# Optimization experiments

Hardware: AMD Instinct MI355X
Metric: run time of the kernel (lower is better)

## Reference

```python
import jax, jax.numpy as jnp
import numpy as np

N = 50000
E = 625000
D_IN, D_HID, D_OUT = 128, 128, 64


def setup_inputs() -> dict:
    key = jax.random.key(0)
    k1, k2, k3, k4 = jax.random.split(key, 4)
    x = jax.random.normal(k1, (N, D_IN), dtype=jnp.float32)
    edge_index = jax.random.randint(k2, (2, E), 0, N, dtype=jnp.int32)
    # Glorot-ish init for linear weights (PyG lin has no bias; bias added after agg)
    W1 = jax.random.normal(k3, (D_HID, D_IN), dtype=jnp.float32) / np.sqrt(D_IN)
    b1 = jnp.zeros((D_HID,), dtype=jnp.float32)
    W2 = jax.random.normal(k4, (D_OUT, D_HID), dtype=jnp.float32) / np.sqrt(D_HID)
    b2 = jnp.zeros((D_OUT,), dtype=jnp.float32)
    return {"x": x, "edge_index": edge_index, "W1": W1, "b1": b1, "W2": W2, "b2": b2}


def _gcn_conv(x, W, b, src, dst, n):
    # GCNConv: h = x @ W^T; out[dst] += norm * h[src]; out += b
    # src/dst already include self-loops; symmetric normalization deg^{-1/2}.
    ones = jnp.ones(src.shape[0], dtype=x.dtype)
    deg = jax.ops.segment_sum(ones, dst, num_segments=n)
    dinv = jnp.where(deg > 0, jax.lax.rsqrt(deg), 0.0)
    norm = dinv[src] * dinv[dst]                      # [E+N]
    h = x @ W.T                                        # [N, d_out]
    msg = norm[:, None] * h[src]                       # [E+N, d_out]
    out = jax.ops.segment_sum(msg, dst, num_segments=n)
    return out + b


def reference(x, edge_index, W1, b1, W2, b2):
    n = x.shape[0]
    loops = jnp.arange(n, dtype=edge_index.dtype)
    src = jnp.concatenate([edge_index[0], loops])      # add self-loops
    dst = jnp.concatenate([edge_index[1], loops])
    h = _gcn_conv(x, W1, b1, src, dst, n)
    h = jax.nn.relu(h)
    out = _gcn_conv(h, W2, b2, src, dst, n)
    return out
```

## Files before the change

### kernel.cpp

```cpp
#include <hip/hip_runtime.h>
#include <hip/hip_bf16.h>


typedef __attribute__((ext_vector_type(8))) __bf16 bf16x8;
typedef __attribute__((ext_vector_type(8))) unsigned short ushort8;
typedef __attribute__((ext_vector_type(4))) float floatx4;

static __device__ __forceinline__ float bf2f(unsigned short s) {
    unsigned u = ((unsigned)s) << 16;
    return __builtin_bit_cast(float, u);
}
static __device__ __forceinline__ unsigned short f2bf(float f) {
    unsigned u = __builtin_bit_cast(unsigned, f);
    unsigned r = (u + 0x7FFFu + ((u >> 16) & 1u)) >> 16;
    return (unsigned short)r;
}
static __device__ __forceinline__ void ld8f(const void* p, size_t idx, int isbf, float* o) {
    if (isbf) {
        ushort8 t = __builtin_bit_cast(ushort8, *(const int4*)((const unsigned short*)p + idx));
        #pragma unroll
        for (int j = 0; j < 8; ++j) o[j] = bf2f(t[j]);
    } else {
        const float* f = (const float*)p + idx;
        float4 a = *(const float4*)f;
        float4 b = *(const float4*)(f + 4);
        o[0]=a.x; o[1]=a.y; o[2]=a.z; o[3]=a.w; o[4]=b.x; o[5]=b.y; o[6]=b.z; o[7]=b.w;
    }
}
static __device__ __forceinline__ int4 ld8frag(const void* p, size_t idx, int isbf) {
    if (isbf) {
        return *(const int4*)((const unsigned short*)p + idx);
    } else {
        const float* f = (const float*)p + idx;
        float4 a = *(const float4*)f;
        float4 b = *(const float4*)(f + 4);
        ushort8 t;
        t[0]=f2bf(a.x); t[1]=f2bf(a.y); t[2]=f2bf(a.z); t[3]=f2bf(a.w);
        t[4]=f2bf(b.x); t[5]=f2bf(b.y); t[6]=f2bf(b.z); t[7]=f2bf(b.w);
        return __builtin_bit_cast(int4, t);
    }
}
static __device__ __forceinline__ float bread(const void* p, int i, int isbf) {
    return isbf ? bf2f(((const unsigned short*)p)[i]) : ((const float*)p)[i];
}

__global__ __launch_bounds__(256) void k_countdet(
    const int* __restrict__ dst, int* __restrict__ cnt, int E, int EB,
    const unsigned* __restrict__ xw, int* __restrict__ flag)
{
    int b = blockIdx.x;
    if (b == EB) {
        __shared__ int red[256];
        int t = threadIdx.x;
        int c = 0;
        #pragma unroll
        for (int i = 0; i < 16; ++i) {
            unsigned w = xw[t * 16 + i];
            unsigned exp = (w >> 7) & 0xFFu;
            c += (exp <= 0x84u) ? 1 : 0;
        }
        red[t] = c;
        __syncthreads();
        for (int s = 128; s > 0; s >>= 1) {
            if (t < s) red[t] += red[t + s];
            __syncthreads();
        }
        if (t == 0) flag[0] = (red[0] >= 3686) ? 1 : 0;
        return;
    }
    int e = b * 256 + threadIdx.x;
    if (e < E) atomicAdd(&cnt[dst[e]], 1);
}

__global__ __launch_bounds__(256) void k_scanA(
    const int* __restrict__ cnt, int* __restrict__ partial, int N)
{
    int b = blockIdx.x, t = threadIdx.x;
    int base = b * 1024 + t * 4;
    int s = 0;
    if (base + 3 < N) {
        int4 v = *(const int4*)&cnt[base];
        s = v.x + v.y + v.z + v.w;
    } else {
        for (int j = 0; j < 4; ++j) { int i = base + j; if (i < N) s += cnt[i]; }
    }
    #pragma unroll
    for (int d = 1; d < 64; d <<= 1) s += __shfl_down(s, d, 64);
    __shared__ int ws[4];
    int lane = t & 63, wid = t >> 6;
    if (lane == 0) ws[wid] = s;
    __syncthreads();
    if (t == 0) partial[b] = ws[0] + ws[1] + ws[2] + ws[3];
}

__global__ __launch_bounds__(256) void k_scanC(
    const int* __restrict__ cnt, const int* __restrict__ partial,
    int* __restrict__ off, int* __restrict__ cursor, float* __restrict__ dinv,
    int N, int nb)
{
    __shared__ int s_pref, s_tot;
    int b = blockIdx.x, t = threadIdx.x, lane = t & 63, wid = t >> 6;
    if (t == 0) {
        int s = 0, pb = 0;
        for (int i = 0; i < nb; ++i) { if (i == b) pb = s; s += partial[i]; }
        s_pref = pb; s_tot = s;
    }
    int base = b * 1024 + t * 4;
    int v[4], s = 0;
    #pragma unroll
    for (int j = 0; j < 4; ++j) {
        int i = base + j;
        v[j] = (i < N) ? cnt[i] : 0;
        s += v[j];
    }
    int x = s;
    #pragma unroll
    for (int d = 1; d < 64; d <<= 1) {
        int u = __shfl_up(x, d, 64);
        if (lane >= d) x += u;
    }
    __shared__ int wtot[4], woff[4];
    if (lane == 63) wtot[wid] = x;
    __syncthreads();
    if (t == 0) {
        int a = 0;
        #pragma unroll
        for (int w = 0; w < 4; ++w) { woff[w] = a; a += wtot[w]; }
    }
    __syncthreads();
    int excl = s_pref + woff[wid] + (x - s);
    #pragma unroll
    for (int j = 0; j < 4; ++j) {
        int i = base + j;
        if (i < N) {
            off[i] = excl;
            cursor[i] = excl;
            dinv[i] = rsqrtf(1.0f + (float)v[j]);
            excl += v[j];
        }
    }
    if (b == 0 && t == 0) off[N] = s_tot;
}

__global__ void k_scatter(const int* __restrict__ src, const int* __restrict__ dst,
                          const float* __restrict__ dinv,
                          int* __restrict__ cursor, int2* __restrict__ bucket, int E) {
    int e = blockIdx.x * 256 + threadIdx.x;
    if (e >= E) return;
    int s = src[e], d = dst[e];
    float w = dinv[s] * dinv[d];
    int pos = atomicAdd(&cursor[d], 1);
    int2 rec; rec.x = s; rec.y = __builtin_bit_cast(int, w);
    bucket[pos] = rec;
}

__global__ __launch_bounds__(256) void k_gather1(
    const void* __restrict__ x, const float* __restrict__ dinv,
    const int* __restrict__ off, const int2* __restrict__ bucket,
    unsigned short* __restrict__ z1, int N, const int* __restrict__ flag)
{
    int isbf = *flag;
    int gid = blockIdx.x * 256 + threadIdx.x;
    int node = gid >> 4, p = gid & 15;
    if (node >= N) return;
    float di = dinv[node];
    float acc[8], va[8], vb[8];
    ld8f(x, (size_t)node * 128 + p * 8, isbf, va);
    float w0 = di * di;
    #pragma unroll
    for (int j = 0; j < 8; ++j) acc[j] = w0 * va[j];
    int it = off[node], s1 = off[node + 1];
    for (; it + 1 < s1; it += 2) {
        int2 ea = bucket[it], eb = bucket[it + 1];
        float wa = __builtin_bit_cast(float, ea.y);
        float wb = __builtin_bit_cast(float, eb.y);
        ld8f(x, (size_t)ea.x * 128 + p * 8, isbf, va);
        ld8f(x, (size_t)eb.x * 128 + p * 8, isbf, vb);
        #pragma unroll
        for (int j = 0; j < 8; ++j) acc[j] += wa * va[j] + wb * vb[j];
    }
    if (it < s1) {
        int2 ea = bucket[it];
        float wa = __builtin_bit_cast(float, ea.y);
        ld8f(x, (size_t)ea.x * 128 + p * 8, isbf, va);
        #pragma unroll
        for (int j = 0; j < 8; ++j) acc[j] += wa * va[j];
    }
    ushort8 o;
    #pragma unroll
    for (int j = 0; j < 8; ++j) o[j] = f2bf(acc[j]);
    *(int4*)&z1[(size_t)node * 128 + p * 8] = __builtin_bit_cast(int4, o);
}

__global__ __launch_bounds__(256) void k_gemm12(
    const unsigned short* __restrict__ z1, const void* __restrict__ W1,
    const void* __restrict__ b1, const void* __restrict__ W2,
    unsigned short* __restrict__ h2, int N, const int* __restrict__ flag)
{
    int isbf = *flag;
    __shared__ int4 w1f[2048];
    __shared__ unsigned short h1t[4][16 * 136];
    int tid = threadIdx.x;
    for (int u = tid; u < 2048; u += 256) {
        int nt = u >> 8, kt = (u >> 6) & 3, lane = u & 63;
        int so = (nt * 16 + (lane & 15)) * 128 + kt * 32 + ((lane >> 4) << 3);
        w1f[u] = ld8frag(W1, so, isbf);
    }
    int wave = tid >> 6, lane = tid & 63, m = lane & 15, quad = lane >> 4;

    int4 w2r[4][4];
    #pragma unroll
    for (int nt = 0; nt < 4; ++nt)
        #pragma unroll
        for (int kt = 0; kt < 4; ++kt)
            w2r[nt][kt] = ld8frag(W2, (nt * 16 + m) * 128 + kt * 32 + quad * 8, isbf);
    __syncthreads();

    int ntile = (N + 15) >> 4;
    int tile = blockIdx.x * 4 + wave;
    int tcl = (tile < ntile) ? tile : (ntile - 1);
    int arow = tcl * 16 + m;
    if (arow >= N) arow = N - 1;

    bf16x8 a[4];
    #pragma unroll
    for (int kt = 0; kt < 4; ++kt)
        a[kt] = __builtin_bit_cast(bf16x8, *(const int4*)&z1[(size_t)arow * 128 + kt * 32 + quad * 8]);
    floatx4 acc[8];
    floatx4 z = {0.f, 0.f, 0.f, 0.f};
    #pragma unroll
    for (int nt = 0; nt < 8; ++nt) acc[nt] = z;
    #pragma unroll
    for (int kt = 0; kt < 4; ++kt)
        #pragma unroll
        for (int nt = 0; nt < 8; ++nt) {
            bf16x8 b = __builtin_bit_cast(bf16x8, w1f[nt * 256 + kt * 64 + lane]);
            acc[nt] = __builtin_amdgcn_mfma_f32_16x16x32_bf16(a[kt], b, acc[nt], 0, 0, 0);
        }
    #pragma unroll
    for (int nt = 0; nt < 8; ++nt) {
        int col = nt * 16 + m;
        float bb = bread(b1, col, isbf);
        #pragma unroll
        for (int r = 0; r < 4; ++r) {
            float v = acc[nt][r] + bb;
            h1t[wave][(quad * 4 + r) * 136 + col] = f2bf(fmaxf(v, 0.f));
        }
    }
    __syncthreads();

    bf16x8 a2[4];
    #pragma unroll
    for (int kt = 0; kt < 4; ++kt)
        a2[kt] = __builtin_bit_cast(bf16x8, *(const int4*)&h1t[wave][m * 136 + kt * 32 + quad * 8]);
    floatx4 acc2[4];
    #pragma unroll
    for (int nt = 0; nt < 4; ++nt) acc2[nt] = z;
    #pragma unroll
    for (int kt = 0; kt < 4; ++kt)
        #pragma unroll
        for (int nt = 0; nt < 4; ++nt) {
            bf16x8 b = __builtin_bit_cast(bf16x8, w2r[nt][kt]);
            acc2[nt] = __builtin_amdgcn_mfma_f32_16x16x32_bf16(a2[kt], b, acc2[nt], 0, 0, 0);
        }
    if (tile < ntile) {
        int rbase = tcl * 16 + quad * 4;
        #pragma unroll
        for (int nt = 0; nt < 4; ++nt) {
            int col = nt * 16 + m;
            #pragma unroll
            for (int r = 0; r < 4; ++r) {
                int orow = rbase + r;
                if (orow < N)
                    h2[(size_t)orow * 64 + col] = f2bf(acc2[nt][r]);
            }
        }
    }
}

__global__ __launch_bounds__(256) void k_gather2(
    const unsigned short* __restrict__ h2, const float* __restrict__ dinv,
    const int* __restrict__ off, const int2* __restrict__ bucket,
    const void* __restrict__ b2, void* __restrict__ out, int N,
    const int* __restrict__ flag)
{
    int isbf = *flag;
    int gid = blockIdx.x * 256 + threadIdx.x;
    int node = gid >> 3, p = gid & 7;
    if (node >= N) return;
    float di = dinv[node];
    float acc[8];
    {
        ushort8 t = __builtin_bit_cast(ushort8, *(const int4*)&h2[(size_t)node * 64 + p * 8]);
        float w0 = di * di;
        #pragma unroll
        for (int j = 0; j < 8; ++j) acc[j] = w0 * bf2f(t[j]);
    }
    int it = off[node], s1 = off[node + 1];
    for (; it + 1 < s1; it += 2) {
        int2 ea = bucket[it], eb = bucket[it + 1];
        float wa = __builtin_bit_cast(float, ea.y);
        float wb = __builtin_bit_cast(float, eb.y);
        ushort8 ta = __builtin_bit_cast(ushort8, *(const int4*)&h2[(size_t)ea.x * 64 + p * 8]);
        ushort8 tb = __builtin_bit_cast(ushort8, *(const int4*)&h2[(size_t)eb.x * 64 + p * 8]);
        #pragma unroll
        for (int j = 0; j < 8; ++j) acc[j] += wa * bf2f(ta[j]) + wb * bf2f(tb[j]);
    }
    if (it < s1) {
        int2 ea = bucket[it];
        float wa = __builtin_bit_cast(float, ea.y);
        ushort8 ta = __builtin_bit_cast(ushort8, *(const int4*)&h2[(size_t)ea.x * 64 + p * 8]);
        #pragma unroll
        for (int j = 0; j < 8; ++j) acc[j] += wa * bf2f(ta[j]);
    }
    #pragma unroll
    for (int j = 0; j < 8; ++j) acc[j] += bread(b2, p * 8 + j, isbf);
    if (isbf) {
        ushort8 o;
        #pragma unroll
        for (int j = 0; j < 8; ++j) o[j] = f2bf(acc[j]);
        *(int4*)((unsigned short*)out + (size_t)node * 64 + p * 8) = __builtin_bit_cast(int4, o);
    } else {
        float* fo = (float*)out + (size_t)node * 64 + p * 8;
        float4 a = {acc[0], acc[1], acc[2], acc[3]};
        float4 b = {acc[4], acc[5], acc[6], acc[7]};
        *(float4*)fo = a;
        *(float4*)(fo + 4) = b;
    }
}

extern "C" void kernel_launch(void* const* d_in, const int* in_sizes, int n_in,
                              void* d_out, int out_size, void* d_ws, size_t ws_size,
                              hipStream_t stream) {
    const void* x  = d_in[0];
    const int*  ei = (const int*)d_in[1];
    const void* W1 = d_in[2];
    const void* b1 = d_in[3];
    const void* W2 = d_in[4];
    const void* b2 = d_in[5];

    int N = in_sizes[0] / 128;
    int E = in_sizes[1] / 2;
    const int* srcI = ei;
    const int* dstI = ei + E;

    int nb = (N + 1023) / 1024;
    int EB = (E + 255) / 256;

    char* base = (char*)d_ws;
    size_t o = 0;
    auto take = [&](size_t bytes) { size_t r = o; o += (bytes + 255) & ~(size_t)255; return r; };
    int*   flag    = (int*)  (base + take(4));
    int*   cnt     = (int*)  (base + take((size_t)N * 4));
    int*   off     = (int*)  (base + take((size_t)(N + 1) * 4));
    int*   cursor  = (int*)  (base + take((size_t)N * 4));
    float* dinv    = (float*)(base + take((size_t)N * 4));
    int*   partial = (int*)  (base + take((size_t)nb * 4));
    int2*  bucket  = (int2*) (base + take((size_t)E * 8));
    unsigned short* z1 = (unsigned short*)(base + take((size_t)N * 128 * 2));
    unsigned short* h2 = (unsigned short*)(base + take((size_t)N * 64 * 2));

    int ntile = (N + 15) / 16;
    int gemmBlocks = (ntile + 3) / 4;

    hipMemsetAsync(cnt, 0, (size_t)N * 4, stream);
    k_countdet<<<EB + 1, 256, 0, stream>>>(dstI, cnt, E, EB, (const unsigned*)x, flag);
    k_scanA<<<nb, 256, 0, stream>>>(cnt, partial, N);
    k_scanC<<<nb, 256, 0, stream>>>(cnt, partial, off, cursor, dinv, N, nb);
    k_scatter<<<EB, 256, 0, stream>>>(srcI, dstI, dinv, cursor, bucket, E);
    k_gather1<<<(N * 16 + 255) / 256, 256, 0, stream>>>(x, dinv, off, bucket, z1, N, flag);
    k_gemm12<<<gemmBlocks, 256, 0, stream>>>(z1, W1, b1, W2, h2, N, flag);
    k_gather2<<<(N * 8 + 255) / 256, 256, 0, stream>>>(h2, dinv, off, bucket, b2, d_out, N, flag);
}
```

Measured before the change: 250.5 us.

## Partially sort CSR neighbor lists by source quartile for gather locality

Counts and bucket positions are now kept per (destination, source-quartile) pair, so each node's neighbor list is grouped into four source-index ranges. The intent is that concurrent gathers across nodes touch nearby source rows at the same time, improving L2 locality for the feature reads in both gather kernels. In exchange the count, offset and cursor arrays grow fourfold, the scan processes four times as many entries, and every edge pays an integer division.

Result: faster. 244.4 us (-2.4%).

```diff
diff --git a/kernel.cpp b/kernel.cpp
--- a/kernel.cpp
+++ b/kernel.cpp
@@ -45,7 +45,8 @@
 }
 
 __global__ __launch_bounds__(256) void k_countdet(
-    const int* __restrict__ dst, int* __restrict__ cnt, int E, int EB,
+    const int* __restrict__ src, const int* __restrict__ dst,
+    int* __restrict__ cnt, int E, int EB, int qdiv,
     const unsigned* __restrict__ xw, int* __restrict__ flag)
 {
     int b = blockIdx.x;
@@ -69,20 +70,24 @@
         return;
     }
     int e = b * 256 + threadIdx.x;
-    if (e < E) atomicAdd(&cnt[dst[e]], 1);
+    if (e < E) {
+        int s = src[e], d = dst[e];
+        int q = s / qdiv; q = (q > 3) ? 3 : q;
+        atomicAdd(&cnt[d * 4 + q], 1);
+    }
 }
 
 __global__ __launch_bounds__(256) void k_scanA(
-    const int* __restrict__ cnt, int* __restrict__ partial, int N)
+    const int* __restrict__ cnt, int* __restrict__ partial, int M)
 {
     int b = blockIdx.x, t = threadIdx.x;
     int base = b * 1024 + t * 4;
     int s = 0;
-    if (base + 3 < N) {
+    if (base + 3 < M) {
         int4 v = *(const int4*)&cnt[base];
         s = v.x + v.y + v.z + v.w;
     } else {
-        for (int j = 0; j < 4; ++j) { int i = base + j; if (i < N) s += cnt[i]; }
+        for (int j = 0; j < 4; ++j) { int i = base + j; if (i < M) s += cnt[i]; }
     }
     #pragma unroll
     for (int d = 1; d < 64; d <<= 1) s += __shfl_down(s, d, 64);
@@ -96,7 +101,7 @@
 __global__ __launch_bounds__(256) void k_scanC(
     const int* __restrict__ cnt, const int* __restrict__ partial,
     int* __restrict__ off, int* __restrict__ cursor, float* __restrict__ dinv,
-    int N, int nb)
+    int M, int nb)
 {
     __shared__ int s_pref, s_tot;
     int b = blockIdx.x, t = threadIdx.x, lane = t & 63, wid = t >> 6;
@@ -110,7 +115,7 @@
     #pragma unroll
     for (int j = 0; j < 4; ++j) {
         int i = base + j;
-        v[j] = (i < N) ? cnt[i] : 0;
+        v[j] = (i < M) ? cnt[i] : 0;
         s += v[j];
     }
     int x = s;
@@ -132,24 +137,29 @@
     #pragma unroll
     for (int j = 0; j < 4; ++j) {
         int i = base + j;
-        if (i < N) {
+        if (i < M) {
             off[i] = excl;
             cursor[i] = excl;
-            dinv[i] = rsqrtf(1.0f + (float)v[j]);
             excl += v[j];
         }
     }
-    if (b == 0 && t == 0) off[N] = s_tot;
+    if (base < M) {
+        int node = base >> 2;
+        dinv[node] = rsqrtf(1.0f + (float)s);
+    }
+    if (b == 0 && t == 0) off[M] = s_tot;
 }
 
 __global__ void k_scatter(const int* __restrict__ src, const int* __restrict__ dst,
                           const float* __restrict__ dinv,
-                          int* __restrict__ cursor, int2* __restrict__ bucket, int E) {
+                          int* __restrict__ cursor, int2* __restrict__ bucket,
+                          int E, int qdiv) {
     int e = blockIdx.x * 256 + threadIdx.x;
     if (e >= E) return;
     int s = src[e], d = dst[e];
+    int q = s / qdiv; q = (q > 3) ? 3 : q;
     float w = dinv[s] * dinv[d];
-    int pos = atomicAdd(&cursor[d], 1);
+    int pos = atomicAdd(&cursor[d * 4 + q], 1);
     int2 rec; rec.x = s; rec.y = __builtin_bit_cast(int, w);
     bucket[pos] = rec;
 }
@@ -169,7 +179,7 @@
     float w0 = di * di;
     #pragma unroll
     for (int j = 0; j < 8; ++j) acc[j] = w0 * va[j];
-    int it = off[node], s1 = off[node + 1];
+    int it = off[node * 4], s1 = off[node * 4 + 4];
     for (; it + 1 < s1; it += 2) {
         int2 ea = bucket[it], eb = bucket[it + 1];
         float wa = __builtin_bit_cast(float, ea.y);
@@ -296,7 +306,7 @@
         #pragma unroll
         for (int j = 0; j < 8; ++j) acc[j] = w0 * bf2f(t[j]);
     }
-    int it = off[node], s1 = off[node + 1];
+    int it = off[node * 4], s1 = off[node * 4 + 4];
     for (; it + 1 < s1; it += 2) {
         int2 ea = bucket[it], eb = bucket[it + 1];
         float wa = __builtin_bit_cast(float, ea.y);
@@ -344,16 +354,18 @@
     const int* srcI = ei;
     const int* dstI = ei + E;
 
-    int nb = (N + 1023) / 1024;
+    int M = N * 4;
+    int qdiv = (N + 3) / 4;
+    int nb = (M + 1023) / 1024;
     int EB = (E + 255) / 256;
 
     char* base = (char*)d_ws;
     size_t o = 0;
     auto take = [&](size_t bytes) { size_t r = o; o += (bytes + 255) & ~(size_t)255; return r; };
     int*   flag    = (int*)  (base + take(4));
-    int*   cnt     = (int*)  (base + take((size_t)N * 4));
-    int*   off     = (int*)  (base + take((size_t)(N + 1) * 4));
-    int*   cursor  = (int*)  (base + take((size_t)N * 4));
+    int*   cnt     = (int*)  (base + take((size_t)M * 4));
+    int*   off     = (int*)  (base + take((size_t)(M + 1) * 4));
+    int*   cursor  = (int*)  (base + take((size_t)M * 4));
     float* dinv    = (float*)(base + take((size_t)N * 4));
     int*   partial = (int*)  (base + take((size_t)nb * 4));
     int2*  bucket  = (int2*) (base + take((size_t)E * 8));
@@ -363,11 +375,11 @@
     int ntile = (N + 15) / 16;
     int gemmBlocks = (ntile + 3) / 4;
 
-    hipMemsetAsync(cnt, 0, (size_t)N * 4, stream);
-    k_countdet<<<EB + 1, 256, 0, stream>>>(dstI, cnt, E, EB, (const unsigned*)x, flag);
-    k_scanA<<<nb, 256, 0, stream>>>(cnt, partial, N);
-    k_scanC<<<nb, 256, 0, stream>>>(cnt, partial, off, cursor, dinv, N, nb);
-    k_scatter<<<EB, 256, 0, stream>>>(srcI, dstI, dinv, cursor, bucket, E);
+    hipMemsetAsync(cnt, 0, (size_t)M * 4, stream);
+    k_countdet<<<EB + 1, 256, 0, stream>>>(srcI, dstI, cnt, E, EB, qdiv, (const unsigned*)x, flag);
+    k_scanA<<<nb, 256, 0, stream>>>(cnt, partial, M);
+    k_scanC<<<nb, 256, 0, stream>>>(cnt, partial, off, cursor, dinv, M, nb);
+    k_scatter<<<EB, 256, 0, stream>>>(srcI, dstI, dinv, cursor, bucket, E, qdiv);
     k_gather1<<<(N * 16 + 255) / 256, 256, 0, stream>>>(x, dinv, off, bucket, z1, N, flag);
     k_gemm12<<<gemmBlocks, 256, 0, stream>>>(z1, W1, b1, W2, h2, N, flag);
     k_gather2<<<(N * 8 + 255) / 256, 256, 0, stream>>>(h2, dinv, off, bucket, b2, d_out, N, flag);
```
